# Performance work log

Measured on AMD Instinct MI355X. Metric: run time of the kernel, lower is better.

## Reference

```python
import jax, jax.numpy as jnp
import numpy as np

B, N, D, E = 128, 512, 256, 8192  # graphs, nodes/graph, embed_dim, edges/graph
K = int(np.ceil(0.8 * N))         # TopKPooling ratio=0.8 -> k per graph


def setup_inputs() -> dict:
    key = jax.random.key(0)
    ks = jax.random.split(key, 16)
    Ntot = B * N
    x = jax.random.normal(ks[0], (Ntot, 4), jnp.float32)
    offs = (jnp.arange(B, dtype=jnp.int32) * N)[:, None]
    src = (jax.random.randint(ks[1], (B, E), 0, N, jnp.int32) + offs).reshape(-1)
    dst = (jax.random.randint(ks[2], (B, E), 0, N, jnp.int32) + offs).reshape(-1)
    s = 0.05
    w = lambda k, shape: jax.random.normal(k, shape, jnp.float32) * s
    return {
        'x': x, 'src': src, 'dst': dst,
        'Wr1': w(ks[3], (4, D)), 'Ws1': w(ks[4], (4, D)), 'b1': jnp.zeros((D,), jnp.float32),
        'Wr2': w(ks[5], (D, D)), 'Ws2': w(ks[6], (D, D)), 'b2': jnp.zeros((D,), jnp.float32),
        'Wr3': w(ks[7], (D, D)), 'Ws3': w(ks[8], (D, D)), 'b3': jnp.zeros((D,), jnp.float32),
        'p_attn': w(ks[9], (D,)),
        'W1': w(ks[10], (2 * D, D)), 'c1': jnp.zeros((D,), jnp.float32),
        'W2': w(ks[11], (D, D // 2)), 'c2': jnp.zeros((D // 2,), jnp.float32),
        'W3': w(ks[12], (D // 2, 1)), 'c3': jnp.zeros((1,), jnp.float32),
    }


def _graph_conv(x, src, dst, Wr, Ws, b):
    # PyG GraphConv, aggr='add': out = lin_rel(sum_{j in N(i)} x_j) + lin_root(x_i)
    agg = jax.ops.segment_sum(x[src], dst, num_segments=B * N)
    return agg @ Wr + b + x @ Ws


def _gmp_gap(xb):
    # xb: [B, n, D] -> concat(global max pool, global mean pool): [B, 2D]
    return jnp.concatenate([xb.max(axis=1), xb.mean(axis=1)], axis=1)


def reference(x, src, dst, Wr1, Ws1, b1, Wr2, Ws2, b2, Wr3, Ws3, b3,
              p_attn, W1, c1, W2, c2, W3, c3):
    h = jax.nn.relu(_graph_conv(x, src, dst, Wr1, Ws1, b1))
    x1 = _gmp_gap(h.reshape(B, N, D))
    h = jax.nn.relu(_graph_conv(h, src, dst, Wr2, Ws2, b2))
    x2 = _gmp_gap(h.reshape(B, N, D))
    h = jax.nn.relu(_graph_conv(h, src, dst, Wr3, Ws3, b3))
    # TopKPooling: score = x.p/||p||; keep top-k per graph; scale by tanh(score)
    score = (h @ p_attn) / (jnp.linalg.norm(p_attn) + 1e-16)
    vals, idx = jax.lax.top_k(score.reshape(B, N), K)           # [B, K]
    hb = h.reshape(B, N, D)
    sel = jnp.take_along_axis(hb, idx[:, :, None], axis=1) * jnp.tanh(vals)[:, :, None]
    x3 = _gmp_gap(sel)
    z = x1 + x2 + x3
    z = jax.nn.relu(z @ W1 + c1)
    z = jax.nn.relu(z @ W2 + c2)  # dropout is identity in eval mode
    return jax.nn.sigmoid(z @ W3 + c3)[:, 0]
```

## Files before the change

### kernel.cpp

```cpp
#include <hip/hip_runtime.h>

typedef unsigned short u16;
typedef unsigned int u32;

#define B_GRAPHS 128
#define N_NODES  512
#define D_DIM    256
#define E_EDGES  8192
#define K_TOP    410
#define CSR_STRIDE 12288

typedef __attribute__((ext_vector_type(8))) __bf16 bf16x8;
typedef __attribute__((ext_vector_type(4))) float  f32x4;

__device__ __forceinline__ float bf2f(u16 h) {
  union { u32 u; float f; } c; c.u = ((u32)h) << 16; return c.f;
}
__device__ __forceinline__ float u2f(u32 u) {
  union { u32 u; float f; } c; c.u = u; return c.f;
}
__device__ __forceinline__ u16 f2bf(float f) {
  union { float f; u32 u; } c; c.f = f;
  u32 u = c.u;
  u += 0x7fffu + ((u >> 16) & 1u);
  return (u16)(u >> 16);
}
__device__ __forceinline__ void async_copy16(const void* g, void* l) {
  __builtin_amdgcn_global_load_lds((const __attribute__((address_space(1))) void*)g,
                                   (__attribute__((address_space(3))) void*)l, 16, 0, 0);
}

__global__ void zero_kernel(float* __restrict__ p) {
  *(float4*)&p[(size_t)(blockIdx.x * 256 + threadIdx.x) * 4] = float4{0.f, 0.f, 0.f, 0.f};
}

__global__ void prep_kernel(const float* __restrict__ Wr2, const float* __restrict__ Ws2,
                            const float* __restrict__ Wr3, const float* __restrict__ Ws3,
                            u16* __restrict__ WT) {
  const int mat = blockIdx.y;
  const int n = blockIdx.x;
  const int k = threadIdx.x;
  const float* W = (mat == 0) ? Wr2 : (mat == 1) ? Ws2 : (mat == 2) ? Wr3 : Ws3;
  WT[((size_t)mat << 16) + ((size_t)n << 8) + k] = f2bf(W[(size_t)k * 256 + n]);
}

__global__ __launch_bounds__(256) void csr_kernel(const int* __restrict__ src,
                                                  const int* __restrict__ dst,
                                                  u16* __restrict__ csr_col,
                                                  u32* __restrict__ csr_off) {
  __shared__ u32 cnt[512];
  __shared__ u32 scan[512];
  __shared__ u32 poff[513];
  const int g = blockIdx.x, t = threadIdx.x;
  const int base = g * N_NODES, ebase = g * E_EDGES;
  for (int i = t; i < 512; i += 256) cnt[i] = 0;
  __syncthreads();
  for (int e = t; e < E_EDGES; e += 256)
    atomicAdd(&cnt[dst[ebase + e] - base], 1u);
  __syncthreads();
  for (int i = t; i < 512; i += 256) scan[i] = (cnt[i] + 7u) & ~7u;
  __syncthreads();
  #pragma unroll 1
  for (int d = 1; d < 512; d <<= 1) {
    const u32 v0 = (t >= d) ? scan[t - d] : 0u;
    const u32 v1 = scan[t + 256 - d];
    __syncthreads();
    if (t >= d) scan[t] += v0;
    scan[t + 256] += v1;
    __syncthreads();
  }
  if (t == 0) poff[0] = 0;
  for (int i = t; i < 512; i += 256) poff[i + 1] = scan[i];
  __syncthreads();
  for (int i = t; i < 513; i += 256) csr_off[(size_t)g * 513 + i] = poff[i];
  for (int i = t; i < 512; i += 256) {
    const u32 s = poff[i] + cnt[i], e2 = poff[i + 1];
    for (u32 k = s; k < e2; ++k) csr_col[(size_t)g * CSR_STRIDE + k] = 16384;
  }
  __syncthreads();
  for (int i = t; i < 512; i += 256) cnt[i] = poff[i];
  __syncthreads();
  for (int e = t; e < E_EDGES; e += 256) {
    const int d = dst[ebase + e] - base;
    const int s = src[ebase + e] - base;
    const u32 pos = atomicAdd(&cnt[d], 1u);
    csr_col[(size_t)g * CSR_STRIDE + pos] = (u16)(s << 5);
  }
}

__global__ __launch_bounds__(256) void conv1_kernel(const float* __restrict__ x,
                             const u16* __restrict__ csr_col, const u32* __restrict__ csr_off,
                             const float* __restrict__ Wr1, const float* __restrict__ Ws1,
                             const float* __restrict__ b1,
                             u16* __restrict__ H1, float* __restrict__ X1) {
  __shared__ float xs[513 * 4];
  __shared__ float aggs[N_NODES * 5];
  __shared__ __align__(16) u16 cols[CSR_STRIDE];
  __shared__ u32 offs[513];
  const int c = blockIdx.x;
  const int g = blockIdx.y;
  const int base = g * N_NODES;
  const int t = threadIdx.x;

  for (int i = t; i < N_NODES; i += 256)
    *(float4*)&xs[i * 4] = *(const float4*)&x[(size_t)(base + i) * 4];
  if (t < 4) xs[512 * 4 + t] = 0.f;
  for (int i = t; i < CSR_STRIDE / 2; i += 256)
    ((u32*)cols)[i] = ((const u32*)(csr_col + (size_t)g * CSR_STRIDE))[i];
  for (int i = t; i < 513; i += 256) offs[i] = csr_off[(size_t)g * 513 + i];
  __syncthreads();

  #pragma unroll
  for (int nn = 0; nn < 2; ++nn) {
    const int i = t * 2 + nn;
    const u32 s0 = offs[i];
    const int nb = (int)((offs[i + 1] - s0) >> 3);
    float a0 = 0.f, a1 = 0.f, a2 = 0.f, a3 = 0.f;
    for (int b = 0; b < nb; ++b) {
      const uint4 cw = *(const uint4*)&cols[s0 + (u32)b * 8];
      const u32 ww[4] = {cw.x, cw.y, cw.z, cw.w};
      #pragma unroll
      for (int q = 0; q < 4; ++q) {
        const int ca = (int)((ww[q] & 0xffffu) >> 5);
        const int cb = (int)(ww[q] >> 21);
        const float4 va = *(const float4*)&xs[ca * 4];
        const float4 vb = *(const float4*)&xs[cb * 4];
        a0 += va.x + vb.x; a1 += va.y + vb.y;
        a2 += va.z + vb.z; a3 += va.w + vb.w;
      }
    }
    aggs[i * 5 + 0] = a0; aggs[i * 5 + 1] = a1;
    aggs[i * 5 + 2] = a2; aggs[i * 5 + 3] = a3;
  }
  __syncthreads();

  float wr[4], wsv[4];
  #pragma unroll
  for (int k = 0; k < 4; ++k) { wr[k] = Wr1[k * 256 + t]; wsv[k] = Ws1[k * 256 + t]; }
  const float bb = b1[t];
  float mx = 0.f, sm = 0.f;
  const int nlo = c * 256;
  for (int n = nlo; n < nlo + 256; ++n) {
    float acc = bb;
    #pragma unroll
    for (int k = 0; k < 4; ++k) acc += aggs[n * 5 + k] * wr[k] + xs[n * 4 + k] * wsv[k];
    acc = fmaxf(acc, 0.f);
    H1[(size_t)(base + n) * D_DIM + t] = f2bf(acc);
    mx = fmaxf(mx, acc);
    sm += acc;
  }
  atomicMax((int*)&X1[(size_t)g * 512 + t], __float_as_int(mx));
  atomicAdd(&X1[(size_t)g * 512 + 256 + t], sm);
}

__global__ __launch_bounds__(512) void agg_gather_kernel(const u16* __restrict__ H,
                                                         const u16* __restrict__ csr_col,
                                                         const u32* __restrict__ csr_off,
                                                         u16* __restrict__ AGG) {
  __shared__ __align__(16) u16 hs[513 * 128];
  __shared__ __align__(16) u16 cols[CSR_STRIDE + 8];
  __shared__ u32 offs[513];
  __shared__ u32 swork[512];
  const int c = blockIdx.x;
  const int g = blockIdx.y;
  const int base = g * N_NODES;
  const int t = threadIdx.x;
  const int w = t >> 6, lane = t & 63;

  {
    const int r0w = w * 64;
    const u16* Hsrc = &H[(size_t)(base + r0w + (lane >> 4)) * D_DIM + c * 128 + (lane & 15) * 8];
    #pragma unroll
    for (int i = 0; i < 16; ++i)
      async_copy16(Hsrc + (size_t)i * 4 * D_DIM, &hs[(r0w + i * 4) * 128]);
    const u16* Csrc = &csr_col[(size_t)g * CSR_STRIDE + w * 1536 + lane * 8];
    #pragma unroll
    for (int i = 0; i < 3; ++i)
      async_copy16(Csrc + i * 512, &cols[(w * 3 + i) * 512]);
  }
  if (t < 32) *(uint2*)&hs[512 * 128 + t * 4] = uint2{0u, 0u};
  if (t < 8) cols[CSR_STRIDE + t] = 16384;
  for (int i = t; i < 513; i += 512) offs[i] = csr_off[(size_t)g * 513 + i];
  asm volatile("s_waitcnt vmcnt(0)" ::: "memory");
  __syncthreads();

  {
    const int row = (w << 6) + lane;
    const u32 s0 = offs[row];
    const u32 nb = (offs[row + 1] - s0) >> 3;
    u32 key = (nb << 16) | (u32)row;
    #pragma unroll
    for (int k = 2; k <= 64; k <<= 1) {
      #pragma unroll
      for (int jj = k >> 1; jj > 0; jj >>= 1) {
        const u32 o = (u32)__shfl_xor((int)key, jj);
        const bool up = ((lane & k) == 0);
        const bool lower = ((lane & jj) == 0);
        const u32 mn = min(key, o), mx = max(key, o);
        key = (up == lower) ? mn : mx;
      }
    }
    swork[(w << 6) + lane] = key;
  }
  __syncthreads();

  const int h2 = lane >> 5, fl = lane & 31;
  const int i0w = w << 6;
  const u32 padu = (u32)(CSR_STRIDE + h2 * 4);
  const u32 h2o = (u32)(h2 * 4);
  #pragma unroll 1
  for (int j = 0; j < 16; ++j) {
    const uint4 kw = *(const uint4*)&swork[i0w + j * 4];
    const int rw[4] = {(int)(kw.x & 0xffffu), (int)(kw.y & 0xffffu),
                       (int)(kw.z & 0xffffu), (int)(kw.w & 0xffffu)};
    const int nb[4] = {(int)(kw.x >> 16), (int)(kw.y >> 16),
                       (int)(kw.z >> 16), (int)(kw.w >> 16)};
    const int nbmax = nb[3];
    u32 cu[4];
    #pragma unroll
    for (int q = 0; q < 4; ++q) cu[q] = offs[rw[q]] + h2o;
    float a[4][4];
    #pragma unroll
    for (int q = 0; q < 4; ++q) { a[q][0] = 0.f; a[q][1] = 0.f; a[q][2] = 0.f; a[q][3] = 0.f; }

    uint2 dA[16], dB[16];
    auto LOAD = [&](uint2 (&d)[16], int b) {
      #pragma unroll
      for (int q = 0; q < 4; ++q) {
        const u32 u = (b < nb[q]) ? (cu[q] + (u32)b * 8u) : padu;
        const uint2 cw = *(const uint2*)&cols[u];
        const int e0 = (int)(cw.x & 0xffffu), e1 = (int)(cw.x >> 16);
        const int e2 = (int)(cw.y & 0xffffu), e3 = (int)(cw.y >> 16);
        d[q * 4 + 0] = *(const uint2*)&hs[(u32)(e0 + fl) << 2];
        d[q * 4 + 1] = *(const uint2*)&hs[(u32)(e1 + fl) << 2];
        d[q * 4 + 2] = *(const uint2*)&hs[(u32)(e2 + fl) << 2];
        d[q * 4 + 3] = *(const uint2*)&hs[(u32)(e3 + fl) << 2];
      }
    };
    auto ACCUM = [&](uint2 (&d)[16]) {
      #pragma unroll
      for (int q = 0; q < 4; ++q) {
        const uint2 d0 = d[q * 4 + 0], d1 = d[q * 4 + 1];
        const uint2 d2 = d[q * 4 + 2], d3 = d[q * 4 + 3];
        a[q][0] += (u2f(d0.x << 16) + u2f(d1.x << 16)) + (u2f(d2.x << 16) + u2f(d3.x << 16));
        a[q][1] += (u2f(d0.x & 0xffff0000u) + u2f(d1.x & 0xffff0000u))
                 + (u2f(d2.x & 0xffff0000u) + u2f(d3.x & 0xffff0000u));
        a[q][2] += (u2f(d0.y << 16) + u2f(d1.y << 16)) + (u2f(d2.y << 16) + u2f(d3.y << 16));
        a[q][3] += (u2f(d0.y & 0xffff0000u) + u2f(d1.y & 0xffff0000u))
                 + (u2f(d2.y & 0xffff0000u) + u2f(d3.y & 0xffff0000u));
      }
    };

    LOAD(dA, 0);
    #pragma unroll 1
    for (int b = 0; b < nbmax; b += 2) {
      if (b + 1 < nbmax) LOAD(dB, b + 1);
      ACCUM(dA);
      if (b + 2 < nbmax) LOAD(dA, b + 2);
      if (b + 1 < nbmax) ACCUM(dB);
    }

    #pragma unroll
    for (int q = 0; q < 4; ++q) {
      const float v0 = a[q][0] + __shfl_xor(a[q][0], 32);
      const float v1 = a[q][1] + __shfl_xor(a[q][1], 32);
      const float v2 = a[q][2] + __shfl_xor(a[q][2], 32);
      const float v3 = a[q][3] + __shfl_xor(a[q][3], 32);
      if (h2 == 0) {
        uint2 o;
        o.x = (u32)f2bf(v0) | ((u32)f2bf(v1) << 16);
        o.y = (u32)f2bf(v2) | ((u32)f2bf(v3) << 16);
        *(uint2*)&AGG[(size_t)(base + rw[q]) * D_DIM + c * 128 + fl * 4] = o;
      }
    }
  }
}

__global__ __launch_bounds__(512) void gemm_kernel(const u16* __restrict__ Amat,
                                                   const u16* __restrict__ Hmat,
                                                   const u16* __restrict__ WrT,
                                                   const u16* __restrict__ WsT,
                                                   const float* __restrict__ bias,
                                                   u16* __restrict__ Hout,
                                                   float* __restrict__ x2pool,
                                                   float* __restrict__ score,
                                                   const float* __restrict__ pvec) {
  __shared__ __align__(16) u16 At[2][256 * 32];
  __shared__ __align__(16) u16 Bt[2][128 * 32];
  const int m0 = blockIdx.x * 256;
  const int n0 = blockIdx.y * 128;
  const int t = threadIdx.x;
  const int wid = t >> 6, lane = t & 63;
  const int wm = wid >> 1, wn = wid & 1;
  const int r16 = lane & 15, q0 = lane >> 4;

  f32x4 acc[4][4];
  const f32x4 zero = {0.f, 0.f, 0.f, 0.f};
  #pragma unroll
  for (int i = 0; i < 4; ++i)
    #pragma unroll
    for (int jj = 0; jj < 4; ++jj) acc[i][jj] = zero;

  const int srow_off = lane >> 2;
  const int sq = lane & 3;

  auto stage = [&](int s) {
    const int buf = s & 1;
    const int ph = s >> 3;
    const int kk = (s & 7) * 32;
    const u16* Ain = ph ? Hmat : Amat;
    const u16* Win = ph ? WsT : WrT;
    #pragma unroll
    for (int j = 0; j < 3; ++j) {
      const int chk = wid * 3 + j;
      if (chk < 16) {
        const int r = chk * 16 + srow_off;
        const int qsrc = sq ^ ((r >> 1) & 3);
        async_copy16(&Ain[(size_t)(m0 + r) * 256 + kk + qsrc * 8], &At[buf][chk * 512]);
      } else {
        const int ch = chk - 16;
        const int r = ch * 16 + srow_off;
        const int qsrc = sq ^ ((r >> 1) & 3);
        async_copy16(&Win[(size_t)(n0 + r) * 256 + kk + qsrc * 8], &Bt[buf][ch * 512]);
      }
    }
  };

  stage(0);
  #pragma unroll 1
  for (int s = 0; s < 16; ++s) {
    if (s < 15) {
      stage(s + 1);
      asm volatile("s_waitcnt vmcnt(3)" ::: "memory");
    } else {
      asm volatile("s_waitcnt vmcnt(0)" ::: "memory");
    }
    __builtin_amdgcn_s_barrier();
    const int buf = s & 1;
    bf16x8 aF[4], bF[4];
    #pragma unroll
    for (int mi = 0; mi < 4; ++mi) {
      const int arow = wm * 64 + mi * 16 + r16;
      const int qs = q0 ^ ((arow >> 1) & 3);
      aF[mi] = *(const bf16x8*)&At[buf][arow * 32 + qs * 8];
    }
    #pragma unroll
    for (int ni = 0; ni < 4; ++ni) {
      const int brow = wn * 64 + ni * 16 + r16;
      const int qs = q0 ^ ((brow >> 1) & 3);
      bF[ni] = *(const bf16x8*)&Bt[buf][brow * 32 + qs * 8];
    }
    #pragma unroll
    for (int mi = 0; mi < 4; ++mi)
      #pragma unroll
      for (int ni = 0; ni < 4; ++ni)
        acc[mi][ni] = __builtin_amdgcn_mfma_f32_16x16x32_bf16(aF[mi], bF[ni],
                                                              acc[mi][ni], 0, 0, 0);
    __builtin_amdgcn_s_barrier();
  }

  const bool do_x2 = (x2pool != nullptr);
  const bool do_sc = (score != nullptr);
  float colmax[4], colsum[4], pv[4], rpart[4][4];
  #pragma unroll
  for (int ni = 0; ni < 4; ++ni) { colmax[ni] = 0.f; colsum[ni] = 0.f; pv[ni] = 0.f; }
  #pragma unroll
  for (int mi = 0; mi < 4; ++mi)
    #pragma unroll
    for (int r = 0; r < 4; ++r) rpart[mi][r] = 0.f;
  if (do_sc) {
    #pragma unroll
    for (int ni = 0; ni < 4; ++ni) pv[ni] = pvec[n0 + wn * 64 + ni * 16 + r16];
  }

  #pragma unroll
  for (int mi = 0; mi < 4; ++mi) {
    const int growb = m0 + wm * 64 + mi * 16 + q0 * 4;
    #pragma unroll
    for (int ni = 0; ni < 4; ++ni) {
      const int gcol = n0 + wn * 64 + ni * 16 + r16;
      const float bv = bias[gcol];
      #pragma unroll
      for (int r = 0; r < 4; ++r) {
        float v = acc[mi][ni][r] + bv;
        v = fmaxf(v, 0.f);
        Hout[(size_t)(growb + r) * 256 + gcol] = f2bf(v);
        colmax[ni] = fmaxf(colmax[ni], v);
        colsum[ni] += v;
        rpart[mi][r] += v * pv[ni];
      }
    }
  }

  const int gg = m0 >> 9;
  if (do_x2) {
    #pragma unroll
    for (int ni = 0; ni < 4; ++ni) {
      const int gcol = n0 + wn * 64 + ni * 16 + r16;
      float cm = colmax[ni], cs = colsum[ni];
      cm = fmaxf(cm, __shfl_xor(cm, 16));
      cm = fmaxf(cm, __shfl_xor(cm, 32));
      cs += __shfl_xor(cs, 16);
      cs += __shfl_xor(cs, 32);
      if (q0 == 0) {
        atomicMax((int*)&x2pool[(size_t)gg * 512 + gcol], __float_as_int(cm));
        atomicAdd(&x2pool[(size_t)gg * 512 + 256 + gcol], cs);
      }
    }
  }
  if (do_sc) {
    #pragma unroll
    for (int mi = 0; mi < 4; ++mi) {
      const int growb = m0 + wm * 64 + mi * 16 + q0 * 4;
      #pragma unroll
      for (int r = 0; r < 4; ++r) {
        float sp = rpart[mi][r];
        sp += __shfl_xor(sp, 1);
        sp += __shfl_xor(sp, 2);
        sp += __shfl_xor(sp, 4);
        sp += __shfl_xor(sp, 8);
        if (r16 == 0) atomicAdd(&score[growb + r], sp);
      }
    }
  }
}

__global__ __launch_bounds__(256) void sort_kernel(const float* __restrict__ score,
                                                   const float* __restrict__ p,
                                                   u16* __restrict__ top_idx,
                                                   float* __restrict__ top_scale) {
  __shared__ float sval[N_NODES];
  __shared__ int sidx[N_NODES];
  __shared__ float wsum[4];
  const int g = blockIdx.x, t = threadIdx.x;

  float pvt = p[t];
  float sq2 = pvt * pvt;
  #pragma unroll
  for (int off = 32; off > 0; off >>= 1) sq2 += __shfl_down(sq2, off);
  if ((t & 63) == 0) wsum[t >> 6] = sq2;
  __syncthreads();
  const float inv_pn = 1.f / (sqrtf(wsum[0] + wsum[1] + wsum[2] + wsum[3]) + 1e-16f);

  for (int n = t; n < N_NODES; n += 256) {
    sval[n] = score[(size_t)g * 512 + n] * inv_pn;
    sidx[n] = n;
  }
  __syncthreads();

  for (int k = 2; k <= N_NODES; k <<= 1) {
    for (int jj = k >> 1; jj > 0; jj >>= 1) {
      const int i = ((t & ~(jj - 1)) << 1) | (t & (jj - 1));
      const int ix = i | jj;
      const bool dirDesc = ((i & k) == 0);
      const float vi = sval[i], vx = sval[ix];
      const int ii = sidx[i], ij = sidx[ix];
      const bool iAfter = (vi < vx) || (vi == vx && ii > ij);
      if (dirDesc ? iAfter : !iAfter) {
        sval[i] = vx; sval[ix] = vi;
        sidx[i] = ij; sidx[ix] = ii;
      }
      __syncthreads();
    }
  }

  for (int s = t; s < K_TOP; s += 256) {
    top_idx[(size_t)g * 416 + s] = (u16)sidx[s];
    top_scale[(size_t)g * 416 + s] = tanhf(sval[s]);
  }
}

__global__ __launch_bounds__(256) void x3_pool_kernel(const u16* __restrict__ H3,
                                                      const u16* __restrict__ top_idx,
                                                      const float* __restrict__ top_scale,
                                                      float* __restrict__ X3) {
  __shared__ u16 sidxL[416];
  __shared__ float ssclL[416];
  __shared__ float redm[32 * 65];
  __shared__ float reds[32 * 65];
  const int c = blockIdx.x;
  const int g = blockIdx.y;
  const int t = threadIdx.x;
  const int fl = t & 7, rg = t >> 3;

  for (int s = t; s < K_TOP; s += 256) {
    sidxL[s] = top_idx[(size_t)g * 416 + s];
    ssclL[s] = top_scale[(size_t)g * 416 + s];
  }
  __syncthreads();

  float mx[8], sm[8];
  #pragma unroll
  for (int j = 0; j < 8; ++j) { mx[j] = -1e30f; sm[j] = 0.f; }
  const size_t rowbase = (size_t)g * 512;
  for (int s = rg; s < K_TOP; s += 32) {
    const int row = sidxL[s];
    const float sc = ssclL[s];
    const uint4 d = *(const uint4*)&H3[(rowbase + row) * 256 + c * 64 + fl * 8];
    const u32 wv[4] = {d.x, d.y, d.z, d.w};
    #pragma unroll
    for (int q = 0; q < 4; ++q) {
      const float v0 = u2f(wv[q] << 16) * sc;
      const float v1 = u2f(wv[q] & 0xffff0000u) * sc;
      mx[q * 2] = fmaxf(mx[q * 2], v0); sm[q * 2] += v0;
      mx[q * 2 + 1] = fmaxf(mx[q * 2 + 1], v1); sm[q * 2 + 1] += v1;
    }
  }
  #pragma unroll
  for (int j = 0; j < 8; ++j) {
    redm[rg * 65 + fl * 8 + j] = mx[j];
    reds[rg * 65 + fl * 8 + j] = sm[j];
  }
  __syncthreads();
  for (int st = 16; st >= 1; st >>= 1) {
    if (rg < st) {
      #pragma unroll
      for (int j = 0; j < 8; ++j) {
        const int a = rg * 65 + fl * 8 + j, b = (rg + st) * 65 + fl * 8 + j;
        redm[a] = fmaxf(redm[a], redm[b]);
        reds[a] += reds[b];
      }
    }
    __syncthreads();
  }
  if (rg == 0) {
    #pragma unroll
    for (int j = 0; j < 8; ++j) {
      X3[(size_t)g * 512 + c * 64 + fl * 8 + j] = redm[fl * 8 + j];
      X3[(size_t)g * 512 + 256 + c * 64 + fl * 8 + j] = reds[fl * 8 + j] * (1.f / (float)K_TOP);
    }
  }
}

__global__ void mlp_kernel(const float* __restrict__ X1, const float* __restrict__ X2,
                           const float* __restrict__ X3,
                           const float* __restrict__ W1, const float* __restrict__ c1,
                           const float* __restrict__ W2, const float* __restrict__ c2,
                           const float* __restrict__ W3, const float* __restrict__ c3,
                           float* __restrict__ out) {
  __shared__ float zs[512];
  __shared__ float z1[256];
  __shared__ float z2[128];
  const int g = blockIdx.x, t = threadIdx.x;
  for (int k = t; k < 512; k += 256) {
    const float x1v = X1[(size_t)g * 512 + k];
    const float x2v = X2[(size_t)g * 512 + k];
    const float x3v = X3[(size_t)g * 512 + k];
    zs[k] = (k < 256) ? (x1v + x2v + x3v)
                      : (x1v * (1.f / 512.f) + x2v * (1.f / 512.f) + x3v);
  }
  __syncthreads();
  {
    float acc = c1[t];
    for (int k = 0; k < 512; ++k) acc += zs[k] * W1[(size_t)k * 256 + t];
    z1[t] = fmaxf(acc, 0.f);
  }
  __syncthreads();
  if (t < 128) {
    float acc = c2[t];
    for (int d = 0; d < 256; ++d) acc += z1[d] * W2[(size_t)d * 128 + t];
    z2[t] = fmaxf(acc, 0.f);
  }
  __syncthreads();
  if (t == 0) {
    float acc = c3[0];
    for (int e = 0; e < 128; ++e) acc += z2[e] * W3[e];
    out[g] = 1.f / (1.f + expf(-acc));
  }
}

extern "C" void kernel_launch(void* const* d_in, const int* in_sizes, int n_in,
                              void* d_out, int out_size, void* d_ws, size_t ws_size,
                              hipStream_t stream) {
  (void)in_sizes; (void)n_in; (void)out_size; (void)ws_size;
  const float* x   = (const float*)d_in[0];
  const int* src   = (const int*)d_in[1];
  const int* dstp  = (const int*)d_in[2];
  const float* Wr1 = (const float*)d_in[3];
  const float* Ws1 = (const float*)d_in[4];
  const float* b1  = (const float*)d_in[5];
  const float* Wr2 = (const float*)d_in[6];
  const float* Ws2 = (const float*)d_in[7];
  const float* b2  = (const float*)d_in[8];
  const float* Wr3 = (const float*)d_in[9];
  const float* Ws3 = (const float*)d_in[10];
  const float* b3  = (const float*)d_in[11];
  const float* pat = (const float*)d_in[12];
  const float* W1  = (const float*)d_in[13];
  const float* c1  = (const float*)d_in[14];
  const float* W2  = (const float*)d_in[15];
  const float* c2  = (const float*)d_in[16];
  const float* W3  = (const float*)d_in[17];
  const float* c3  = (const float*)d_in[18];
  float* out = (float*)d_out;

  char* ws = (char*)d_ws;
  u16* hA  = (u16*)(ws);
  u16* hB  = (u16*)(ws + 33554432);
  u16* AGG = (u16*)(ws + 67108864);
  u16* WT  = (u16*)(ws + 100663296);
  float* x1 = (float*)(ws + 101187584);
  float* x2 = (float*)(ws + 101449728);
  float* x3 = (float*)(ws + 101711872);
  u16* csr_col = (u16*)(ws + 101974016);
  u32* csr_off = (u32*)(ws + 105119744);
  float* score     = (float*)(ws + 101974016);
  u16* top_idx     = (u16*)(ws + 101974016 + 262144);
  float* top_scale = (float*)(ws + 101974016 + 372736);

  prep_kernel<<<dim3(256, 4), dim3(256), 0, stream>>>(Wr2, Ws2, Wr3, Ws3, WT);
  csr_kernel<<<dim3(128), dim3(256), 0, stream>>>(src, dstp, csr_col, csr_off);
  zero_kernel<<<dim3(128), dim3(256), 0, stream>>>(x1);
  conv1_kernel<<<dim3(2, 128), dim3(256), 0, stream>>>(x, csr_col, csr_off, Wr1, Ws1, b1, hA, x1);

  agg_gather_kernel<<<dim3(2, 128), dim3(512), 0, stream>>>(hA, csr_col, csr_off, AGG);
  gemm_kernel<<<dim3(256, 2), dim3(512), 0, stream>>>(AGG, hA, WT, WT + 65536, b2, hB,
                                                      x2, nullptr, nullptr);

  agg_gather_kernel<<<dim3(2, 128), dim3(512), 0, stream>>>(hB, csr_col, csr_off, AGG);
  zero_kernel<<<dim3(64), dim3(256), 0, stream>>>(score);
  gemm_kernel<<<dim3(256, 2), dim3(512), 0, stream>>>(AGG, hB, WT + 131072, WT + 196608, b3, hA,
                                                      nullptr, score, pat);

  sort_kernel<<<dim3(128), dim3(256), 0, stream>>>(score, pat, top_idx, top_scale);
  x3_pool_kernel<<<dim3(4, 128), dim3(256), 0, stream>>>(hA, top_idx, top_scale, x3);
  mlp_kernel<<<dim3(128), dim3(256), 0, stream>>>(x1, x2, x3, W1, c1, W2, c2, W3, c3, out);
}
```

Measured before the change: 252.8 us.

## Replace CSR gather aggregation with dense per-graph adjacency MFMA matmul

```diff
diff --git a/kernel.cpp b/kernel.cpp
--- a/kernel.cpp
+++ b/kernel.cpp
@@ -85,6 +85,40 @@
     const int s = src[ebase + e] - base;
     const u32 pos = atomicAdd(&cnt[d], 1u);
     csr_col[(size_t)g * CSR_STRIDE + pos] = (u16)(s << 5);
+  }
+}
+
+__global__ __launch_bounds__(512) void build_a_kernel(const u16* __restrict__ csr_col,
+                                                      const u32* __restrict__ csr_off,
+                                                      u32* __restrict__ A4) {
+  __shared__ unsigned char cnt8[128 * 512];
+  __shared__ __align__(16) u16 colsL[CSR_STRIDE];
+  const int c = blockIdx.x, g = blockIdx.y;
+  const int t = threadIdx.x;
+  #pragma unroll
+  for (int i = 0; i < 8; ++i)
+    ((uint4*)cnt8)[i * 512 + t] = uint4{0u, 0u, 0u, 0u};
+  for (int i = t; i < CSR_STRIDE / 2; i += 512)
+    ((u32*)colsL)[i] = ((const u32*)(csr_col + (size_t)g * CSR_STRIDE))[i];
+  __syncthreads();
+  if (t < 128) {
+    const int row = c * 128 + t;
+    const u32 s0 = csr_off[(size_t)g * 513 + row];
+    const u32 s1 = csr_off[(size_t)g * 513 + row + 1];
+    for (u32 k = s0; k < s1; ++k) {
+      const int col = colsL[k] >> 5;
+      if (col < 512) cnt8[t * 512 + col]++;
+    }
+  }
+  __syncthreads();
+  u32* outp = A4 + (size_t)(g * 512 + c * 128) * 64;
+  for (int i = t; i < 8192; i += 512) {
+    const u32 lo = ((const u32*)cnt8)[i * 2];
+    const u32 hi = ((const u32*)cnt8)[i * 2 + 1];
+    const u32 a = lo | (lo >> 4);
+    const u32 b = hi | (hi >> 4);
+    outp[i] = (a & 0xffu) | ((a >> 8) & 0xff00u) | ((b << 16) & 0xff0000u)
+            | ((b << 8) & 0xff000000u);
   }
 }
 
@@ -153,125 +187,105 @@
   atomicAdd(&X1[(size_t)g * 512 + 256 + t], sm);
 }
 
-__global__ __launch_bounds__(512) void agg_gather_kernel(const u16* __restrict__ H,
-                                                         const u16* __restrict__ csr_col,
-                                                         const u32* __restrict__ csr_off,
-                                                         u16* __restrict__ AGG) {
-  __shared__ __align__(16) u16 hs[513 * 128];
-  __shared__ __align__(16) u16 cols[CSR_STRIDE + 8];
-  __shared__ u32 offs[513];
-  __shared__ u32 swork[512];
-  const int c = blockIdx.x;
-  const int g = blockIdx.y;
-  const int base = g * N_NODES;
+__device__ __forceinline__ bf16x8 decode_a4(u32 a) {
+  union { u32 w[4]; bf16x8 v; } r;
+  #pragma unroll
+  for (int p = 0; p < 4; ++p) {
+    const float f0 = (float)((a >> (8 * p)) & 15u);
+    const float f1 = (float)((a >> (8 * p + 4)) & 15u);
+    r.w[p] = (__float_as_uint(f0) >> 16) | (__float_as_uint(f1) & 0xffff0000u);
+  }
+  return r.v;
+}
+
+__global__ __launch_bounds__(512) void agg_mfma_kernel(const u16* __restrict__ H,
+                                                       const u32* __restrict__ A4,
+                                                       u16* __restrict__ AGG) {
+  __shared__ __align__(16) u16 HtL[8192];
+  const int bid = blockIdx.x;
+  const int lb = (bid >> 3) + (bid & 7) * 64;
+  const int g = lb >> 2, cdst = lb & 3;
+  const int gbase = g * 512;
+  const int dstbase = cdst * 128;
   const int t = threadIdx.x;
   const int w = t >> 6, lane = t & 63;
-
-  {
-    const int r0w = w * 64;
-    const u16* Hsrc = &H[(size_t)(base + r0w + (lane >> 4)) * D_DIM + c * 128 + (lane & 15) * 8];
-    #pragma unroll
-    for (int i = 0; i < 16; ++i)
-      async_copy16(Hsrc + (size_t)i * 4 * D_DIM, &hs[(r0w + i * 4) * 128]);
-    const u16* Csrc = &csr_col[(size_t)g * CSR_STRIDE + w * 1536 + lane * 8];
-    #pragma unroll
-    for (int i = 0; i < 3; ++i)
-      async_copy16(Csrc + i * 512, &cols[(w * 3 + i) * 512]);
-  }
-  if (t < 32) *(uint2*)&hs[512 * 128 + t * 4] = uint2{0u, 0u};
-  if (t < 8) cols[CSR_STRIDE + t] = 16384;
-  for (int i = t; i < 513; i += 512) offs[i] = csr_off[(size_t)g * 513 + i];
-  asm volatile("s_waitcnt vmcnt(0)" ::: "memory");
-  __syncthreads();
-
-  {
-    const int row = (w << 6) + lane;
-    const u32 s0 = offs[row];
-    const u32 nb = (offs[row + 1] - s0) >> 3;
-    u32 key = (nb << 16) | (u32)row;
-    #pragma unroll
-    for (int k = 2; k <= 64; k <<= 1) {
-      #pragma unroll
-      for (int jj = k >> 1; jj > 0; jj >>= 1) {
-        const u32 o = (u32)__shfl_xor((int)key, jj);
-        const bool up = ((lane & k) == 0);
-        const bool lower = ((lane & jj) == 0);
-        const u32 mn = min(key, o), mx = max(key, o);
-        key = (up == lower) ? mn : mx;
-      }
-    }
-    swork[(w << 6) + lane] = key;
-  }
-  __syncthreads();
-
-  const int h2 = lane >> 5, fl = lane & 31;
-  const int i0w = w << 6;
-  const u32 padu = (u32)(CSR_STRIDE + h2 * 4);
-  const u32 h2o = (u32)(h2 * 4);
+  const int wm = w >> 2, wf = w & 3;
+  const int r16 = lane & 15, gq = lane >> 4;
+
+  const int oct = t >> 4, sp = t & 15;
+  const u16* Hg = H + (size_t)gbase * 256;
+  const size_t goff = (size_t)(2 * sp) * 256 + oct * 8;
+  const int so = (sp >> 2) ^ (oct & 3);
+  int wb[4];
+  #pragma unroll
+  for (int k = 0; k < 4; ++k) wb[k] = oct * 512 + (sp & 3) * 4 + ((so ^ k) << 4);
+
+  const int subE = gq ^ ((r16 >> 1) & 3) ^ (r16 >> 3);
+  const int rbE = wf * 4096 + r16 * 64 + (subE << 4);
+  const int rbO = wf * 4096 + r16 * 64 + ((subE ^ 2) << 4);
+
+  const u32* Ap = A4 + (size_t)(g * 512 + dstbase + wm * 64 + r16) * 64 + gq;
+
+  f32x4 acc[4][4];
+  const f32x4 zero = {0.f, 0.f, 0.f, 0.f};
+  #pragma unroll
+  for (int mi = 0; mi < 4; ++mi)
+    #pragma unroll
+    for (int ft = 0; ft < 4; ++ft) acc[mi][ft] = zero;
+
+  uint4 rA = *(const uint4*)&Hg[goff];
+  uint4 rB = *(const uint4*)&Hg[goff + 256];
+  uint4 rAn, rBn;
+
   #pragma unroll 1
-  for (int j = 0; j < 16; ++j) {
-    const uint4 kw = *(const uint4*)&swork[i0w + j * 4];
-    const int rw[4] = {(int)(kw.x & 0xffffu), (int)(kw.y & 0xffffu),
-                       (int)(kw.z & 0xffffu), (int)(kw.w & 0xffffu)};
-    const int nb[4] = {(int)(kw.x >> 16), (int)(kw.y >> 16),
-                       (int)(kw.z >> 16), (int)(kw.w >> 16)};
-    const int nbmax = nb[3];
-    u32 cu[4];
-    #pragma unroll
-    for (int q = 0; q < 4; ++q) cu[q] = offs[rw[q]] + h2o;
-    float a[4][4];
-    #pragma unroll
-    for (int q = 0; q < 4; ++q) { a[q][0] = 0.f; a[q][1] = 0.f; a[q][2] = 0.f; a[q][3] = 0.f; }
-
-    uint2 dA[16], dB[16];
-    auto LOAD = [&](uint2 (&d)[16], int b) {
-      #pragma unroll
-      for (int q = 0; q < 4; ++q) {
-        const u32 u = (b < nb[q]) ? (cu[q] + (u32)b * 8u) : padu;
-        const uint2 cw = *(const uint2*)&cols[u];
-        const int e0 = (int)(cw.x & 0xffffu), e1 = (int)(cw.x >> 16);
-        const int e2 = (int)(cw.y & 0xffffu), e3 = (int)(cw.y >> 16);
-        d[q * 4 + 0] = *(const uint2*)&hs[(u32)(e0 + fl) << 2];
-        d[q * 4 + 1] = *(const uint2*)&hs[(u32)(e1 + fl) << 2];
-        d[q * 4 + 2] = *(const uint2*)&hs[(u32)(e2 + fl) << 2];
-        d[q * 4 + 3] = *(const uint2*)&hs[(u32)(e3 + fl) << 2];
-      }
-    };
-    auto ACCUM = [&](uint2 (&d)[16]) {
-      #pragma unroll
-      for (int q = 0; q < 4; ++q) {
-        const uint2 d0 = d[q * 4 + 0], d1 = d[q * 4 + 1];
-        const uint2 d2 = d[q * 4 + 2], d3 = d[q * 4 + 3];
-        a[q][0] += (u2f(d0.x << 16) + u2f(d1.x << 16)) + (u2f(d2.x << 16) + u2f(d3.x << 16));
-        a[q][1] += (u2f(d0.x & 0xffff0000u) + u2f(d1.x & 0xffff0000u))
-                 + (u2f(d2.x & 0xffff0000u) + u2f(d3.x & 0xffff0000u));
-        a[q][2] += (u2f(d0.y << 16) + u2f(d1.y << 16)) + (u2f(d2.y << 16) + u2f(d3.y << 16));
-        a[q][3] += (u2f(d0.y & 0xffff0000u) + u2f(d1.y & 0xffff0000u))
-                 + (u2f(d2.y & 0xffff0000u) + u2f(d3.y & 0xffff0000u));
-      }
-    };
-
-    LOAD(dA, 0);
-    #pragma unroll 1
-    for (int b = 0; b < nbmax; b += 2) {
-      if (b + 1 < nbmax) LOAD(dB, b + 1);
-      ACCUM(dA);
-      if (b + 2 < nbmax) LOAD(dA, b + 2);
-      if (b + 1 < nbmax) ACCUM(dB);
-    }
-
-    #pragma unroll
-    for (int q = 0; q < 4; ++q) {
-      const float v0 = a[q][0] + __shfl_xor(a[q][0], 32);
-      const float v1 = a[q][1] + __shfl_xor(a[q][1], 32);
-      const float v2 = a[q][2] + __shfl_xor(a[q][2], 32);
-      const float v3 = a[q][3] + __shfl_xor(a[q][3], 32);
-      if (h2 == 0) {
-        uint2 o;
-        o.x = (u32)f2bf(v0) | ((u32)f2bf(v1) << 16);
-        o.y = (u32)f2bf(v2) | ((u32)f2bf(v3) << 16);
-        *(uint2*)&AGG[(size_t)(base + rw[q]) * D_DIM + c * 128 + fl * 4] = o;
-      }
+  for (int st = 0; st < 16; ++st) {
+    {
+      const u32 wa[4] = {rA.x, rA.y, rA.z, rA.w};
+      const u32 wbv[4] = {rB.x, rB.y, rB.z, rB.w};
+      #pragma unroll
+      for (int p = 0; p < 4; ++p) {
+        const u32 ve = (wa[p] & 0xffffu) | (wbv[p] << 16);
+        const u32 vo = (wa[p] >> 16) | (wbv[p] & 0xffff0000u);
+        *(u32*)((char*)HtL + wb[p] + (2 * p) * 64) = ve;
+        *(u32*)((char*)HtL + wb[p] + (2 * p + 1) * 64) = vo;
+      }
+    }
+    asm volatile("s_waitcnt lgkmcnt(0)" ::: "memory");
+    __builtin_amdgcn_s_barrier();
+
+    if (st < 15) {
+      const size_t noff = goff + (size_t)(st + 1) * 32 * 256;
+      rAn = *(const uint4*)&Hg[noff];
+      rBn = *(const uint4*)&Hg[noff + 256];
+    }
+
+    bf16x8 aF[4];
+    #pragma unroll
+    for (int mi = 0; mi < 4; ++mi) aF[mi] = decode_a4(Ap[mi * 1024 + st * 4]);
+    bf16x8 bF[4];
+    bF[0] = *(const bf16x8*)((const char*)HtL + rbE);
+    bF[1] = *(const bf16x8*)((const char*)HtL + rbO + 1024);
+    bF[2] = *(const bf16x8*)((const char*)HtL + rbE + 2048);
+    bF[3] = *(const bf16x8*)((const char*)HtL + rbO + 3072);
+    #pragma unroll
+    for (int mi = 0; mi < 4; ++mi)
+      #pragma unroll
+      for (int ft = 0; ft < 4; ++ft)
+        acc[mi][ft] = __builtin_amdgcn_mfma_f32_16x16x32_bf16(aF[mi], bF[ft],
+                                                              acc[mi][ft], 0, 0, 0);
+    __builtin_amdgcn_s_barrier();
+    rA = rAn; rB = rBn;
+  }
+
+  #pragma unroll
+  for (int mi = 0; mi < 4; ++mi) {
+    const size_t rowb = (size_t)(gbase + dstbase + wm * 64 + mi * 16 + gq * 4) * 256;
+    #pragma unroll
+    for (int ft = 0; ft < 4; ++ft) {
+      const int col = wf * 64 + ft * 16 + r16;
+      #pragma unroll
+      for (int r = 0; r < 4; ++r)
+        AGG[rowb + (size_t)r * 256 + col] = f2bf(acc[mi][ft][r]);
     }
   }
 }
@@ -604,6 +618,7 @@
   float* x3 = (float*)(ws + 101711872);
   u16* csr_col = (u16*)(ws + 101974016);
   u32* csr_off = (u32*)(ws + 105119744);
+  u32* A4u     = (u32*)(ws + 105383936);
   float* score     = (float*)(ws + 101974016);
   u16* top_idx     = (u16*)(ws + 101974016 + 262144);
   float* top_scale = (float*)(ws + 101974016 + 372736);
@@ -611,13 +626,14 @@
   prep_kernel<<<dim3(256, 4), dim3(256), 0, stream>>>(Wr2, Ws2, Wr3, Ws3, WT);
   csr_kernel<<<dim3(128), dim3(256), 0, stream>>>(src, dstp, csr_col, csr_off);
   zero_kernel<<<dim3(128), dim3(256), 0, stream>>>(x1);
+  build_a_kernel<<<dim3(4, 128), dim3(512), 0, stream>>>(csr_col, csr_off, A4u);
   conv1_kernel<<<dim3(2, 128), dim3(256), 0, stream>>>(x, csr_col, csr_off, Wr1, Ws1, b1, hA, x1);
 
-  agg_gather_kernel<<<dim3(2, 128), dim3(512), 0, stream>>>(hA, csr_col, csr_off, AGG);
+  agg_mfma_kernel<<<dim3(512), dim3(512), 0, stream>>>(hA, A4u, AGG);
   gemm_kernel<<<dim3(256, 2), dim3(512), 0, stream>>>(AGG, hA, WT, WT + 65536, b2, hB,
                                                       x2, nullptr, nullptr);
 
-  agg_gather_kernel<<<dim3(2, 128), dim3(512), 0, stream>>>(hB, csr_col, csr_off, AGG);
+  agg_mfma_kernel<<<dim3(512), dim3(512), 0, stream>>>(hB, A4u, AGG);
   zero_kernel<<<dim3(64), dim3(256), 0, stream>>>(score);
   gemm_kernel<<<dim3(256, 2), dim3(512), 0, stream>>>(AGG, hB, WT + 131072, WT + 196608, b3, hA,
                                                       nullptr, score, pat);
```

Measured after the change: 278.4 us. 10.1% more time.
